# Optimization experiments

Hardware: AMD Instinct MI355X
Metric: run time of the kernel (lower is better)

Reference implementation:

```python
import jax, jax.numpy as jnp
import numpy as np

IN_DIM = 128
HID = 64  # hidden_dim
N_NODES = 100000
N_EDGES = 1000000

def setup_inputs() -> dict:
    key = jax.random.key(0)
    ks = jax.random.split(key, 8)
    z = jax.random.normal(ks[0], (N_NODES, IN_DIM), dtype=jnp.float32)
    edge_index = jax.random.randint(ks[1], (2, N_EDGES), 0, N_NODES, dtype=jnp.int64)
    # MLP params: Linear(2*in_dim, hid) -> ReLU -> Linear(hid, hid//2) -> ReLU -> Linear(hid//2, 1)
    def lin(k, fan_in, fan_out):
        bound = 1.0 / np.sqrt(fan_in)
        kw, kb = jax.random.split(k)
        W = jax.random.uniform(kw, (fan_in, fan_out), minval=-bound, maxval=bound, dtype=jnp.float32)
        b = jax.random.uniform(kb, (fan_out,), minval=-bound, maxval=bound, dtype=jnp.float32)
        return W, b
    W1, b1 = lin(ks[2], 2 * IN_DIM, HID)
    W2, b2 = lin(ks[3], HID, HID // 2)
    W3, b3 = lin(ks[4], HID // 2, 1)
    return {"z": z, "edge_index": edge_index, "W1": W1, "b1": b1, "W2": W2, "b2": b2, "W3": W3, "b3": b3}

def reference(z, edge_index, W1, b1, W2, b2, W3, b3):
    # gather endpoint embeddings: [E, in_dim] each
    zi = z[edge_index[0]]
    zj = z[edge_index[1]]
    h = jnp.concatenate([zi, zj], axis=-1)          # [E, 2*in_dim]
    h = jax.nn.relu(h @ W1 + b1)                     # [E, hid] (dropout = identity in eval)
    h = jax.nn.relu(h @ W2 + b2)                     # [E, hid//2]
    logits = (h @ W3 + b3).squeeze(-1)               # [E]
    return jax.nn.sigmoid(logits)
```

## Files before the change

kernel.cpp:

```cpp
#include <hip/hip_runtime.h>
#include <hip/hip_bf16.h>

typedef __attribute__((ext_vector_type(8))) short short8;
typedef __attribute__((ext_vector_type(4))) float f32x4;
typedef __attribute__((ext_vector_type(2))) float f32x2;

__device__ __forceinline__ unsigned short f32_bf16(float f) {
  unsigned u = __float_as_uint(f);
  u += 0x7fffu + ((u >> 16) & 1u);
  return (unsigned short)(u >> 16);
}

__device__ __forceinline__ unsigned cvt_pk_bf16(float lo, float hi) {
  unsigned r;
  asm("v_cvt_pk_bf16_f32 %0, %1, %2" : "=v"(r) : "v"(lo), "v"(hi));
  return r;
}

__device__ __forceinline__ short8 cvt8(float4 v0, float4 v1) {
  union { unsigned u[4]; short8 s; } f;
  f.u[0] = cvt_pk_bf16(v0.x, v0.y);
  f.u[1] = cvt_pk_bf16(v0.z, v0.w);
  f.u[2] = cvt_pk_bf16(v1.x, v1.y);
  f.u[3] = cvt_pk_bf16(v1.z, v1.w);
  return f.s;
}

template <int CTRL>
__device__ __forceinline__ float dpp_add(float x) {
  int y = __builtin_amdgcn_update_dpp(0, __float_as_int(x), CTRL, 0xf, 0xf, true);
  return x + __int_as_float(y);
}
__device__ __forceinline__ float row_sum16(float x) {
  x = dpp_add<0x118>(x);
  x = dpp_add<0x114>(x);
  x = dpp_add<0x112>(x);
  x = dpp_add<0x111>(x);
  return x;
}


__global__ __launch_bounds__(256, 2) void uv_kernel(
    const float* __restrict__ z, const float* __restrict__ W1,
    const float* __restrict__ b1,
    unsigned char* __restrict__ uv, int nNodes) {
  __shared__ unsigned short w1l[32 * 64 * 8];
  const int tid = threadIdx.x;
  const int wv  = tid >> 6;
  const int l   = tid & 63;
  const int l15 = l & 15;
  const int q   = l >> 4;

#pragma unroll
  for (int pp = 0; pp < 8; ++pp) {
    int p = wv * 8 + pp;
    int c = p >> 3, t = p & 7;
    int n = ((l15 >= 8) ? 64 : 0) + ((t & 1) << 5) + (((l15 & 7) >> 1) << 3)
            + ((l15 & 1) << 2) + (t >> 1);
    short8 f;
#pragma unroll
    for (int j = 0; j < 8; ++j) {
      int k = c * 32 + q * 8 + j;
      int row = (n < 64) ? k : (k + 128);
      f[j] = (short)f32_bf16(W1[row * 64 + (n & 63)]);
    }
    *(short8*)(w1l + (p * 64 + l) * 8) = f;
  }
  float b1v[8];
#pragma unroll
  for (int j = 0; j < 8; ++j) {
    int n = ((j & 1) << 5) + (((l15 & 7) >> 1) << 3) + ((l15 & 1) << 2) + (j >> 1);
    b1v[j] = (l15 < 8) ? b1[n] : 0.f;
  }
  __syncthreads();

  const int nTiles = (nNodes + 15) >> 4;
  const int stride = gridDim.x * 4;
  for (int tile = blockIdx.x * 4 + wv; tile < nTiles; tile += stride) {
    int node = tile * 16 + l15;
    node = node < nNodes ? node : nNodes - 1;
    const float* zr = z + (size_t)node * 128;
    short8 a[4];
#pragma unroll
    for (int c = 0; c < 4; ++c) {
      int off = c * 32 + q * 8;
      a[c] = cvt8(*(const float4*)(zr + off), *(const float4*)(zr + off + 4));
    }
    f32x4 acc[8];
#pragma unroll
    for (int t = 0; t < 8; ++t) { acc[t][0] = 0.f; acc[t][1] = 0.f; acc[t][2] = 0.f; acc[t][3] = 0.f; }
#pragma unroll
    for (int c = 0; c < 4; ++c)
#pragma unroll
      for (int t = 0; t < 8; ++t) {
        short8 wf = *(const short8*)(w1l + ((c * 8 + t) * 64 + l) * 8);
        acc[t] = __builtin_amdgcn_mfma_f32_16x16x32_bf16(a[c], wf, acc[t], 0, 0, 0);
      }
#pragma unroll
    for (int r = 0; r < 4; ++r) {
      int no = tile * 16 + q * 4 + r;
      if (no < nNodes) {
        float v0 = acc[0][r] + b1v[0], v1 = acc[1][r] + b1v[1];
        float v2 = acc[2][r] + b1v[2], v3 = acc[3][r] + b1v[3];
        float v4 = acc[4][r] + b1v[4], v5 = acc[5][r] + b1v[5];
        float v6 = acc[6][r] + b1v[6], v7 = acc[7][r] + b1v[7];
        unsigned w0 = (unsigned)__builtin_amdgcn_cvt_pk_fp8_f32(v0, v1, 0, false);
        w0 = (unsigned)__builtin_amdgcn_cvt_pk_fp8_f32(v2, v3, (int)w0, true);
        unsigned w1 = (unsigned)__builtin_amdgcn_cvt_pk_fp8_f32(v4, v5, 0, false);
        w1 = (unsigned)__builtin_amdgcn_cvt_pk_fp8_f32(v6, v7, (int)w1, true);
        uint2 pk; pk.x = w0; pk.y = w1;
        *(uint2*)(uv + (size_t)no * 128 + l15 * 8) = pk;
      }
    }
  }
}

__global__ __launch_bounds__(256, 8) void lp_edge(
    const unsigned char* __restrict__ uv, const int* __restrict__ ei,
    const float* __restrict__ W2, const float* __restrict__ b2,
    const float* __restrict__ W3, const float* __restrict__ b3,
    float* __restrict__ out, int nEdges) {
  const int tid = threadIdx.x;
  const int wv  = tid >> 6;
  const int l   = tid & 63;
  const int l15 = l & 15;
  const int q   = l >> 4;

  short8 w2f[2][2];
#pragma unroll
  for (int c = 0; c < 2; ++c)
#pragma unroll
    for (int t = 0; t < 2; ++t) {
      short8 f;
#pragma unroll
      for (int j = 0; j < 8; ++j)
        f[j] = (short)f32_bf16(W2[(c * 32 + q * 8 + j) * 32 + (t * 16 + l15)]);
      w2f[c][t] = f;
    }
  float bb2[2];
#pragma unroll
  for (int t = 0; t < 2; ++t) bb2[t] = b2[t * 16 + l15];
  const float w3a = W3[l15], w3b = W3[16 + l15], b3v = b3[0];

  const unsigned q16 = (unsigned)q * 16u;

  const int nIter = (nEdges + 15) >> 4;
  const int stride = gridDim.x * 4;
  const int it0 = blockIdx.x * 4 + wv;

  int e0 = it0 * 16 + l15; e0 = e0 < nEdges ? e0 : nEdges - 1;
  int cS = __builtin_nontemporal_load(ei + e0);
  int cD = __builtin_nontemporal_load(ei + nEdges + e0);

  for (int iter = it0; iter < nIter; iter += stride) {
    unsigned offU = ((unsigned)cS << 7) + q16;
    unsigned offV = ((unsigned)cD << 7) + 64u + q16;
    uint4 uu = *(const uint4*)(uv + offU);
    uint4 vv = *(const uint4*)(uv + offV);

    int nit = iter + stride;
    if (nit < nIter) {
      int e = nit * 16 + l15;
      e = e < nEdges ? e : nEdges - 1;
      cS = __builtin_nontemporal_load(ei + e);
      cD = __builtin_nontemporal_load(ei + nEdges + e);
    }

    union { unsigned u[4]; short8 s; } f0, f1;
    unsigned uw[4] = {uu.x, uu.y, uu.z, uu.w};
    unsigned vw[4] = {vv.x, vv.y, vv.z, vv.w};
#pragma unroll
    for (int k = 0; k < 4; ++k) {
      f32x2 ua = __builtin_amdgcn_cvt_pk_f32_fp8((int)uw[k], false);
      f32x2 ub = __builtin_amdgcn_cvt_pk_f32_fp8((int)uw[k], true);
      f32x2 va = __builtin_amdgcn_cvt_pk_f32_fp8((int)vw[k], false);
      f32x2 vb = __builtin_amdgcn_cvt_pk_f32_fp8((int)vw[k], true);
      float s0a = ua.x + va.x; s0a = s0a > 0.f ? s0a : 0.f;
      float s1a = ua.y + va.y; s1a = s1a > 0.f ? s1a : 0.f;
      float s0b = ub.x + vb.x; s0b = s0b > 0.f ? s0b : 0.f;
      float s1b = ub.y + vb.y; s1b = s1b > 0.f ? s1b : 0.f;
      f0.u[k] = cvt_pk_bf16(s0a, s0b);
      f1.u[k] = cvt_pk_bf16(s1a, s1b);
    }

    f32x4 acc2[2];
#pragma unroll
    for (int t = 0; t < 2; ++t) {
      acc2[t][0] = bb2[t]; acc2[t][1] = bb2[t]; acc2[t][2] = bb2[t]; acc2[t][3] = bb2[t];
    }
#pragma unroll
    for (int t = 0; t < 2; ++t) {
      acc2[t] = __builtin_amdgcn_mfma_f32_16x16x32_bf16(f0.s, w2f[0][t], acc2[t], 0, 0, 0);
      acc2[t] = __builtin_amdgcn_mfma_f32_16x16x32_bf16(f1.s, w2f[1][t], acc2[t], 0, 0, 0);
    }

    float p[4];
#pragma unroll
    for (int r = 0; r < 4; ++r) {
      float h0 = acc2[0][r]; h0 = h0 > 0.f ? h0 : 0.f;
      float h1v = acc2[1][r]; h1v = h1v > 0.f ? h1v : 0.f;
      p[r] = row_sum16(h0 * w3a + h1v * w3b);
    }

    if (l15 == 15) {
      int eb = iter * 16 + q * 4;
      f32x4 o;
      o[0] = 1.f / (1.f + __expf(-(p[0] + b3v)));
      o[1] = 1.f / (1.f + __expf(-(p[1] + b3v)));
      o[2] = 1.f / (1.f + __expf(-(p[2] + b3v)));
      o[3] = 1.f / (1.f + __expf(-(p[3] + b3v)));
      if (eb + 3 < nEdges) {
        __builtin_nontemporal_store(o, (f32x4*)(out + eb));
      } else {
        if (eb < nEdges)     out[eb]     = o[0];
        if (eb + 1 < nEdges) out[eb + 1] = o[1];
        if (eb + 2 < nEdges) out[eb + 2] = o[2];
      }
    }
  }
}

__global__ void lp_naive(const float* __restrict__ z, const int* __restrict__ ei,
                         const float* __restrict__ W1, const float* __restrict__ b1,
                         const float* __restrict__ W2, const float* __restrict__ b2,
                         const float* __restrict__ W3, const float* __restrict__ b3,
                         float* __restrict__ out, int nEdges) {
  int e = blockIdx.x * 256 + threadIdx.x;
  if (e >= nEdges) return;
  int s = ei[e], d = ei[nEdges + e];
  float h1[64], h2[32];
  for (int k = 0; k < 64; ++k) {
    float a = b1[k];
    for (int i = 0; i < 128; ++i) a += z[(size_t)s * 128 + i] * W1[i * 64 + k];
    for (int i = 0; i < 128; ++i) a += z[(size_t)d * 128 + i] * W1[(128 + i) * 64 + k];
    h1[k] = a > 0.f ? a : 0.f;
  }
  for (int k = 0; k < 32; ++k) {
    float a = b2[k];
    for (int i = 0; i < 64; ++i) a += h1[i] * W2[i * 32 + k];
    h2[k] = a > 0.f ? a : 0.f;
  }
  float lg = b3[0];
  for (int i = 0; i < 32; ++i) lg += h2[i] * W3[i];
  out[e] = 1.f / (1.f + __expf(-lg));
}

extern "C" void kernel_launch(void* const* d_in, const int* in_sizes, int n_in,
                              void* d_out, int out_size, void* d_ws, size_t ws_size,
                              hipStream_t stream) {
  const float* z  = (const float*)d_in[0];
  const int* ei   = (const int*)d_in[1];
  const float* W1 = (const float*)d_in[2];
  const float* b1 = (const float*)d_in[3];
  const float* W2 = (const float*)d_in[4];
  const float* b2 = (const float*)d_in[5];
  const float* W3 = (const float*)d_in[6];
  const float* b3 = (const float*)d_in[7];
  float* out = (float*)d_out;

  const int nZ = in_sizes[0];
  const int nNodes = nZ / 128;
  const int nEdges = in_sizes[1] / 2;

  if (ws_size >= (size_t)nNodes * 128) {
    unsigned char* uvp = (unsigned char*)d_ws;
    int nTiles = (nNodes + 15) >> 4;
    int uvGrid = (nTiles + 3) >> 2;
    if (uvGrid > 2048) uvGrid = 2048;
    uv_kernel<<<uvGrid, 256, 0, stream>>>(z, W1, b1, uvp, nNodes);
    lp_edge<<<2048, 256, 0, stream>>>(uvp, ei, W2, b2, W3, b3, out, nEdges);
  } else {
    lp_naive<<<(nEdges + 255) / 256, 256, 0, stream>>>(z, ei, W1, b1, W2, b2, W3, b3, out, nEdges);
  }
}
```

Measured before the change: 136.9 us.

## Software-pipeline node loads and edge gathers one iteration ahead

In the node projection kernel, the next tile's z rows are prefetched with nontemporal loads while the current tile's MFMAs run, and the occupancy hint rises from 2 to 4 blocks. In the edge kernel, the gathered uv rows for the next iteration and the edge indices two iterations ahead are loaded before the current iteration's work, hiding gather latency. Scheduling barriers hold the loads in place. This increases register pressure, which may conflict with the higher occupancy target.

Measured after the change: 142.6 us. 1.04x slower.

```diff
diff --git a/kernel.cpp b/kernel.cpp
--- a/kernel.cpp
+++ b/kernel.cpp
@@ -17,12 +17,12 @@
   return r;
 }
 
-__device__ __forceinline__ short8 cvt8(float4 v0, float4 v1) {
+__device__ __forceinline__ short8 cvt8(f32x4 v0, f32x4 v1) {
   union { unsigned u[4]; short8 s; } f;
-  f.u[0] = cvt_pk_bf16(v0.x, v0.y);
-  f.u[1] = cvt_pk_bf16(v0.z, v0.w);
-  f.u[2] = cvt_pk_bf16(v1.x, v1.y);
-  f.u[3] = cvt_pk_bf16(v1.z, v1.w);
+  f.u[0] = cvt_pk_bf16(v0[0], v0[1]);
+  f.u[1] = cvt_pk_bf16(v0[2], v0[3]);
+  f.u[2] = cvt_pk_bf16(v1[0], v1[1]);
+  f.u[3] = cvt_pk_bf16(v1[2], v1[3]);
   return f.s;
 }
 
@@ -40,7 +40,7 @@
 }
 
 
-__global__ __launch_bounds__(256, 2) void uv_kernel(
+__global__ __launch_bounds__(256, 4) void uv_kernel(
     const float* __restrict__ z, const float* __restrict__ W1,
     const float* __restrict__ b1,
     unsigned char* __restrict__ uv, int nNodes) {
@@ -76,16 +76,38 @@
 
   const int nTiles = (nNodes + 15) >> 4;
   const int stride = gridDim.x * 4;
-  for (int tile = blockIdx.x * 4 + wv; tile < nTiles; tile += stride) {
+  int tile = blockIdx.x * 4 + wv;
+
+  f32x4 r[8];
+  if (tile < nTiles) {
     int node = tile * 16 + l15;
     node = node < nNodes ? node : nNodes - 1;
-    const float* zr = z + (size_t)node * 128;
+    const f32x4* zr = (const f32x4*)(z + (size_t)node * 128);
+#pragma unroll
+    for (int c = 0; c < 4; ++c) {
+      r[2 * c]     = __builtin_nontemporal_load(zr + c * 8 + q * 2);
+      r[2 * c + 1] = __builtin_nontemporal_load(zr + c * 8 + q * 2 + 1);
+    }
+  }
+
+  for (; tile < nTiles; tile += stride) {
     short8 a[4];
 #pragma unroll
-    for (int c = 0; c < 4; ++c) {
-      int off = c * 32 + q * 8;
-      a[c] = cvt8(*(const float4*)(zr + off), *(const float4*)(zr + off + 4));
-    }
+    for (int c = 0; c < 4; ++c) a[c] = cvt8(r[2 * c], r[2 * c + 1]);
+
+    int nt = tile + stride;
+    if (nt < nTiles) {
+      int node = nt * 16 + l15;
+      node = node < nNodes ? node : nNodes - 1;
+      const f32x4* zr = (const f32x4*)(z + (size_t)node * 128);
+#pragma unroll
+      for (int c = 0; c < 4; ++c) {
+        r[2 * c]     = __builtin_nontemporal_load(zr + c * 8 + q * 2);
+        r[2 * c + 1] = __builtin_nontemporal_load(zr + c * 8 + q * 2 + 1);
+      }
+    }
+    __builtin_amdgcn_sched_barrier(0);
+
     f32x4 acc[8];
 #pragma unroll
     for (int t = 0; t < 8; ++t) { acc[t][0] = 0.f; acc[t][1] = 0.f; acc[t][2] = 0.f; acc[t][3] = 0.f; }
@@ -97,13 +119,13 @@
         acc[t] = __builtin_amdgcn_mfma_f32_16x16x32_bf16(a[c], wf, acc[t], 0, 0, 0);
       }
 #pragma unroll
-    for (int r = 0; r < 4; ++r) {
-      int no = tile * 16 + q * 4 + r;
+    for (int rr = 0; rr < 4; ++rr) {
+      int no = tile * 16 + q * 4 + rr;
       if (no < nNodes) {
-        float v0 = acc[0][r] + b1v[0], v1 = acc[1][r] + b1v[1];
-        float v2 = acc[2][r] + b1v[2], v3 = acc[3][r] + b1v[3];
-        float v4 = acc[4][r] + b1v[4], v5 = acc[5][r] + b1v[5];
-        float v6 = acc[6][r] + b1v[6], v7 = acc[7][r] + b1v[7];
+        float v0 = acc[0][rr] + b1v[0], v1 = acc[1][rr] + b1v[1];
+        float v2 = acc[2][rr] + b1v[2], v3 = acc[3][rr] + b1v[3];
+        float v4 = acc[4][rr] + b1v[4], v5 = acc[5][rr] + b1v[5];
+        float v6 = acc[6][rr] + b1v[6], v7 = acc[7][rr] + b1v[7];
         unsigned w0 = (unsigned)__builtin_amdgcn_cvt_pk_fp8_f32(v0, v1, 0, false);
         w0 = (unsigned)__builtin_amdgcn_cvt_pk_fp8_f32(v2, v3, (int)w0, true);
         unsigned w1 = (unsigned)__builtin_amdgcn_cvt_pk_fp8_f32(v4, v5, 0, false);
@@ -151,20 +173,27 @@
   int e0 = it0 * 16 + l15; e0 = e0 < nEdges ? e0 : nEdges - 1;
   int cS = __builtin_nontemporal_load(ei + e0);
   int cD = __builtin_nontemporal_load(ei + nEdges + e0);
-
-  for (int iter = it0; iter < nIter; iter += stride) {
+  uint4 uu, vv;
+  {
     unsigned offU = ((unsigned)cS << 7) + q16;
     unsigned offV = ((unsigned)cD << 7) + 64u + q16;
-    uint4 uu = *(const uint4*)(uv + offU);
-    uint4 vv = *(const uint4*)(uv + offV);
-
-    int nit = iter + stride;
-    if (nit < nIter) {
-      int e = nit * 16 + l15;
-      e = e < nEdges ? e : nEdges - 1;
-      cS = __builtin_nontemporal_load(ei + e);
-      cD = __builtin_nontemporal_load(ei + nEdges + e);
-    }
+    uu = *(const uint4*)(uv + offU);
+    vv = *(const uint4*)(uv + offV);
+  }
+  int e1 = (it0 + stride) * 16 + l15; e1 = e1 < nEdges ? e1 : nEdges - 1;
+  int nS = __builtin_nontemporal_load(ei + e1);
+  int nD = __builtin_nontemporal_load(ei + nEdges + e1);
+
+  for (int iter = it0; iter < nIter; iter += stride) {
+    unsigned offU = ((unsigned)nS << 7) + q16;
+    unsigned offV = ((unsigned)nD << 7) + 64u + q16;
+    uint4 bu = *(const uint4*)(uv + offU);
+    uint4 bv = *(const uint4*)(uv + offV);
+    __builtin_amdgcn_sched_barrier(0);
+
+    int e2 = (iter + 2 * stride) * 16 + l15; e2 = e2 < nEdges ? e2 : nEdges - 1;
+    nS = __builtin_nontemporal_load(ei + e2);
+    nD = __builtin_nontemporal_load(ei + nEdges + e2);
 
     union { unsigned u[4]; short8 s; } f0, f1;
     unsigned uw[4] = {uu.x, uu.y, uu.z, uu.w};
@@ -217,6 +246,8 @@
         if (eb + 2 < nEdges) out[eb + 2] = o[2];
       }
     }
+
+    uu = bu; vv = bv;
   }
 }
 
```
